# Kernel tuning notes

Hardware: AMD Instinct MI355X
Metric: run time of the kernel (lower is better)

Reference implementation:

```python
import jax, jax.numpy as jnp
import numpy as np

ALPHA = 0.5      # APPNP teleport prob (AG_EAGCN alpha=0.5)
DEPTH = 3        # APPNP depth
PROP_NUMS = 3    # EAGCN propagation steps


def _adj_process(adj, eps):
    # adj[adj<eps]=0 ; symmetrize ; add I ; D^-1/2 A D^-1/2 (inf->0)
    N = adj.shape[1]
    adj = jnp.where(adj < eps, 0.0, adj)
    adj = 0.5 * (adj + jnp.swapaxes(adj, 1, 2))
    adj = adj + jnp.eye(N, dtype=adj.dtype)
    d = jnp.sum(adj, axis=2)                                   # [n, N]
    dinv = jnp.where(d > 0, 1.0 / jnp.sqrt(jnp.where(d > 0, d, 1.0)), 0.0)
    return adj * dinv[:, :, None] * dinv[:, None, :]


def _eagcn(seg, edge, ws1, bs1, ws11, bs11, ws2, bs2, ws3, bs3, wmlp, bmlp, wgcn, bgcn):
    n, c, h, w = seg.shape
    hw = h * w
    num_s = ws1.shape[0]
    # conv_s1 (1x1)
    seg_s = jnp.einsum('nchw,sc->nshw', seg, ws1) + bs1[None, :, None, None]
    theta_T = seg_s.reshape(n, num_s, hw)       # raw view, as in torch
    theta = seg_s.reshape(n, hw, num_s)         # raw view (NOT transpose)
    # channel attention: diag_channel_att = ca ca^T is rank-1 ->
    # theta @ (ca ca^T) @ theta_T = (theta@ca) outer (ca@theta_T)
    pooled = seg.mean(axis=(2, 3))                              # [n, c]
    ca = jax.nn.relu(pooled @ wmlp.T + bmlp)                    # [n, num_s]
    u = jnp.einsum('nps,ns->np', theta, ca)                     # [n, hw]
    v = jnp.einsum('ns,nsq->nq', ca, theta_T)                   # [n, hw]
    sim_c = _adj_process(u[:, :, None] * v[:, None, :], 0.15)
    # spatial branch
    seg_c = jnp.einsum('nchw,sc->nshw', seg, ws11) + bs11[None, :, None, None]
    sigma = seg_c.reshape(n, num_s, hw)
    sigma_T = seg_c.reshape(n, hw, num_s)
    sigma_out = jnp.einsum('nps,nsq->npq', sigma_T, sigma)      # [n, hw, hw]
    edge_m = seg * edge
    seg_ss = (ws2 * seg.max(axis=1) + bs2).reshape(n, 1, hw)    # 1x1 conv on 1 chan
    edge_mm = (ws3 * edge_m.max(axis=1) + bs3).reshape(n, hw, 1)
    sim_s = _adj_process(sigma_out * (edge_mm * seg_ss), 0.15)
    sim = _adj_process(sim_c + sim_s, 0.0)
    # GCN_layer: relu(conv1d(seg @ sim)) + seg, residual
    seg2 = seg.reshape(n, c, hw)
    seg_sim = jnp.einsum('nck,nkq->ncq', seg2, sim)
    out = jax.nn.relu(jnp.einsum('oc,ncq->noq', wgcn, seg_sim) + bgcn[None, :, None]) + seg2
    return out.reshape(n, c, h, w), sim


def _appnp(seg, adj, wa1, ba1, wa2, ba2):
    n, c, h, w = seg.shape
    x = seg.reshape(n, h * w, c)                                # raw view
    t = jax.nn.relu(jax.nn.relu(x @ wa1.T + ba1) @ wa2.T + ba2)
    out = t
    for _ in range(DEPTH):
        out = (1.0 - ALPHA) * jnp.einsum('npq,nqc->npc', adj, out) + ALPHA * t
    return out


def _forward(seg, edge, ws1, bs1, ws11, bs11, ws2, bs2, ws3, bs3,
             wmlp, bmlp, wgcn, bgcn, wa1, ba1, wa2, ba2):
    ori = seg
    n, c, h, w = seg.shape
    adjs = []
    for _ in range(PROP_NUMS):
        seg, adj = _eagcn(seg, edge, ws1, bs1, ws11, bs11, ws2, bs2, ws3, bs3,
                          wmlp, bmlp, wgcn, bgcn)
        adjs.append(adj)
    adj = (adjs[0] + adjs[1] + adjs[2]) / float(PROP_NUMS)      # mean aggregation
    adj = _adj_process(adj, 0.0)
    # graph regularizer
    dirichlet = jnp.einsum('nii->', adj)                        # sum of traces
    N = adj.shape[1]
    gamma = 0.1; beta = 0.1; alpha_r = 0.1
    rowsum = jnp.sum(adj, axis=2)                               # adj @ ones
    f_A = (-beta * jnp.sum(jnp.log(rowsum), axis=1)[:, None, None] / N
           + gamma * jnp.sqrt(jnp.sum(adj * adj)) / (N ** 2))
    reg = alpha_r * dirichlet + f_A                             # [n,1,1]
    out = _appnp(ori, adj, wa1, ba1, wa2, ba2).reshape(n, c, h, w)
    return out, reg


def setup_inputs() -> dict:
    key = jax.random.key(0)
    ks = jax.random.split(key, 10)
    n, c, h, w = 8, 256, 32, 32
    num_s, hid = 64, 3

    def lin(k, out_f, in_f):
        lim = 1.0 / np.sqrt(in_f)
        return jax.random.uniform(k, (out_f, in_f), jnp.float32, -lim, lim)

    return dict(
        seg=jax.random.normal(ks[0], (n, c, h, w), jnp.float32),
        edge=jax.random.uniform(ks[1], (n, c, h, w), jnp.float32),
        ws1=lin(ks[2], num_s, c), bs1=jnp.zeros((num_s,), jnp.float32),
        ws11=lin(ks[3], num_s, c), bs11=jnp.zeros((num_s,), jnp.float32),
        ws2=jnp.asarray(0.7, jnp.float32), bs2=jnp.asarray(0.1, jnp.float32),
        ws3=jnp.asarray(0.6, jnp.float32), bs3=jnp.asarray(0.1, jnp.float32),
        wmlp=lin(ks[4], num_s, c), bmlp=jnp.zeros((num_s,), jnp.float32),
        wgcn=lin(ks[5], c, c), bgcn=jnp.zeros((c,), jnp.float32),
        wa1=lin(ks[6], hid, c), ba1=jnp.zeros((hid,), jnp.float32),
        wa2=lin(ks[7], c, hid), ba2=jnp.zeros((c,), jnp.float32),
    )


def reference(seg, edge, ws1, bs1, ws11, bs11, ws2, bs2, ws3, bs3,
              wmlp, bmlp, wgcn, bgcn, wa1, ba1, wa2, ba2):
    return _forward(seg, edge, ws1, bs1, ws11, bs11, ws2, bs2, ws3, bs3,
                    wmlp, bmlp, wgcn, bgcn, wa1, ba1, wa2, ba2)
```

## Files before the change

kernel.cpp:

```cpp
#include <hip/hip_runtime.h>
#include <math.h>

#define NB 8
#define C 256
#define HW 1024
#define NS 64

typedef unsigned short u16;
typedef __attribute__((ext_vector_type(8))) short bf16x8;
typedef __attribute__((ext_vector_type(4))) float f32x4;

__device__ __forceinline__ u16 f2bf(float x) {
    union { float f; unsigned u; } v; v.f = x;
    unsigned r = v.u + 0x7fffu + ((v.u >> 16) & 1u);
    return (u16)(r >> 16);
}
__device__ __forceinline__ float bf2f(u16 h) {
    union { unsigned u; float f; } v; v.u = ((unsigned)h) << 16; return v.f;
}
__device__ __forceinline__ void splitbf(float x, u16& h, u16& l) {
    h = f2bf(x);
    l = f2bf(x - bf2f(h));
}

__device__ __forceinline__ float blockReduceSum(float v, float* s4) {
    #pragma unroll
    for (int o = 32; o; o >>= 1) v += __shfl_down(v, o);
    __syncthreads();
    if ((threadIdx.x & 63) == 0) s4[threadIdx.x >> 6] = v;
    __syncthreads();
    return s4[0] + s4[1] + s4[2] + s4[3];
}

__global__ void k_presplit(const float* __restrict__ in, u16* __restrict__ oh,
                           u16* __restrict__ ol, int nElem) {
    for (int i = blockIdx.x * 256 + threadIdx.x; i < nElem; i += gridDim.x * 256) {
        u16 h, l; splitbf(in[i], h, l);
        oh[i] = h; ol[i] = l;
    }
}

__global__ void k_prepw(const float* __restrict__ ws1, const float* __restrict__ bs1,
                        const float* __restrict__ ws11, const float* __restrict__ bs11,
                        u16* __restrict__ WCH, u16* __restrict__ WCL, float* __restrict__ BCAT) {
    int tid = blockIdx.x * 256 + threadIdx.x;
    if (tid < 64 * C) {
        u16 h, l;
        splitbf(ws1[tid], h, l);  WCH[tid] = h;          WCL[tid] = l;
        splitbf(ws11[tid], h, l); WCH[64 * C + tid] = h; WCL[64 * C + tid] = l;
    }
    if (tid < 64) { BCAT[tid] = bs1[tid]; BCAT[64 + tid] = bs11[tid]; }
}

template<int R, int CIN, bool WF32>
__global__ void k_transp_split(const float* __restrict__ in, long long sIn,
                               u16* __restrict__ oh, u16* __restrict__ ol,
                               float* __restrict__ of, long long sOut) {
    int ti = blockIdx.x, tj = blockIdx.y, n = blockIdx.z, tid = threadIdx.x;
    int i0 = ti * 64, j0 = tj * 64;
    const float* ib = in + (size_t)n * sIn;
    __shared__ float L[64][65];
    for (int idx = tid; idx < 4096; idx += 256) {
        int r = idx >> 6, c = idx & 63;
        L[r][c] = ib[(size_t)(i0 + r) * CIN + (j0 + c)];
    }
    __syncthreads();
    for (int idx = tid; idx < 4096; idx += 256) {
        int r = idx >> 6, c = idx & 63;
        size_t o = (size_t)n * sOut + (size_t)(j0 + r) * R + (i0 + c);
        float val = L[c][r];
        u16 h, l; splitbf(val, h, l);
        oh[o] = h; ol[o] = l;
        if (WF32) of[o] = val;
    }
}

__global__ void k_pooled(const float* __restrict__ seg, float* __restrict__ pooled) {
    int c = blockIdx.x, n = blockIdx.y, tid = threadIdx.x;
    const float* row = seg + ((size_t)n * C + c) * HW;
    float acc = row[tid] + row[tid + 256] + row[tid + 512] + row[tid + 768];
    __shared__ float s4[4];
    float r = blockReduceSum(acc, s4);
    if (tid == 0) pooled[n * C + c] = r * (1.0f / HW);
}

__global__ void k_ca(const float* __restrict__ pooled, const float* __restrict__ wmlp,
                     const float* __restrict__ bmlp, float* __restrict__ ca) {
    int n = blockIdx.x, s = threadIdx.x;
    __shared__ float pl[C];
    for (int i = s; i < C; i += 64) pl[i] = pooled[n * C + i];
    __syncthreads();
    float acc = 0.f;
    for (int c = 0; c < C; ++c) acc += pl[c] * wmlp[s * C + c];
    float r = acc + bmlp[s];
    ca[n * NS + s] = r > 0.f ? r : 0.f;
}

__global__ void k_maxes(const float* __restrict__ seg, const float* __restrict__ edge,
                        float* __restrict__ smax, float* __restrict__ emax) {
    int pos = blockIdx.x * 256 + threadIdx.x;
    int n = blockIdx.y, ch = blockIdx.z;
    const float* sb = seg + (size_t)n * C * HW + (size_t)(ch * 32) * HW + pos;
    const float* eb = edge + (size_t)n * C * HW + (size_t)(ch * 32) * HW + pos;
    float ms = -3.402823466e38f, me = -3.402823466e38f;
    #pragma unroll 8
    for (int c = 0; c < 32; ++c) {
        float s = sb[(size_t)c * HW];
        ms = fmaxf(ms, s);
        me = fmaxf(me, s * eb[(size_t)c * HW]);
    }
    smax[((size_t)ch * NB + n) * HW + pos] = ms;
    emax[((size_t)ch * NB + n) * HW + pos] = me;
}

__global__ void k_maxfin(const float* __restrict__ smax, const float* __restrict__ emax,
                         const float* __restrict__ ws2, const float* __restrict__ bs2,
                         const float* __restrict__ ws3, const float* __restrict__ bs3,
                         float* __restrict__ segss, float* __restrict__ edgemm) {
    int pos = blockIdx.x * 256 + threadIdx.x;
    int n = blockIdx.y;
    float ms = -3.402823466e38f, me = -3.402823466e38f;
    #pragma unroll
    for (int ch = 0; ch < 8; ++ch) {
        ms = fmaxf(ms, smax[((size_t)ch * NB + n) * HW + pos]);
        me = fmaxf(me, emax[((size_t)ch * NB + n) * HW + pos]);
    }
    segss[n * HW + pos] = ws2[0] * ms + bs2[0];
    edgemm[n * HW + pos] = ws3[0] * me + bs3[0];
}

__global__ void k_uv(const float* __restrict__ segsc, const float* __restrict__ ca,
                     float* __restrict__ u, float* __restrict__ vv) {
    int pos = blockIdx.x * 256 + threadIdx.x;
    int n = blockIdx.y, role = blockIdx.z;
    const float* flat = segsc + (size_t)n * 128 * HW;
    __shared__ float cs[NS];
    if (threadIdx.x < NS) cs[threadIdx.x] = ca[n * NS + threadIdx.x];
    __syncthreads();
    if (role == 0) {
        const float* base = flat + (size_t)pos * NS;
        float acc = 0.f;
        #pragma unroll
        for (int s = 0; s < NS; ++s) acc += base[s] * cs[s];
        u[n * HW + pos] = acc;
    } else {
        float acc = 0.f;
        #pragma unroll
        for (int s = 0; s < NS; ++s) acc += cs[s] * flat[(size_t)s * HW + pos];
        vv[n * HW + pos] = acc;
    }
}

__global__ __launch_bounds__(256) void k_bbuild(
    const u16* __restrict__ AH, const u16* __restrict__ AL, long long sA,
    const u16* __restrict__ CTH, const u16* __restrict__ CTL, long long sCT,
    const float* __restrict__ em, const float* __restrict__ ss,
    float* __restrict__ B, float* __restrict__ dsum) {
    constexpr int LDK = 72;
    constexpr int TSZ = 64 * LDK;
    __shared__ __align__(16) u16 sm[4 * 2 * TSZ];
    int pi = blockIdx.x, n = blockIdx.y, tid = threadIdx.x;
    int i = 0, base = 0;
    while (pi >= base + (16 - i)) { base += 16 - i; ++i; }
    int j = i + (pi - base);
    int i0 = i * 64, j0 = j * 64;
    bool diag = (i == j);
    const u16* AnH = AH + (size_t)n * sA;
    const u16* AnL = AL + (size_t)n * sA;
    const u16* CnH = CTH + (size_t)n * sCT;
    const u16* CnL = CTL + (size_t)n * sCT;
    const float* emn = em + n * HW;
    const float* ssn = ss + n * HW;
    float* Bn = B + (size_t)n * HW * HW;

    auto stage = [&](int t, const u16* srcH, const u16* srcL, int r0) {
        u16* hi = sm + t * 2 * TSZ;
        u16* lo = hi + TSZ;
        #pragma unroll
        for (int p = 0; p < 2; ++p) {
            int e = (p * 256 + tid) * 8;
            int r = e >> 6, k0 = e & 63;
            size_t off = (size_t)(r0 + r) * 64 + k0;
            int b = r * LDK + k0;
            *(bf16x8*)(hi + b) = *(const bf16x8*)(srcH + off);
            *(bf16x8*)(lo + b) = *(const bf16x8*)(srcL + off);
        }
    };
    stage(0, AnH, AnL, i0);
    stage(2, CnH, CnL, i0);
    if (!diag) { stage(1, AnH, AnL, j0); stage(3, CnH, CnL, j0); }
    __syncthreads();

    int lane = tid & 63, wv = tid >> 6;
    int g = lane >> 4;
    f32x4 acc1[4], acc2[4];
    #pragma unroll
    for (int ni = 0; ni < 4; ++ni) {
        acc1[ni] = (f32x4){0.f, 0.f, 0.f, 0.f};
        acc2[ni] = (f32x4){0.f, 0.f, 0.f, 0.f};
    }

    const u16* AiH = sm + 0 * 2 * TSZ; const u16* AiL = AiH + TSZ;
    const u16* AjH = sm + 1 * 2 * TSZ; const u16* AjL = AjH + TSZ;
    const u16* BiH = sm + 2 * 2 * TSZ; const u16* BiL = BiH + TSZ;
    const u16* BjH = sm + 3 * 2 * TSZ; const u16* BjL = BjH + TSZ;

    #pragma unroll
    for (int kk = 0; kk < 2; ++kk) {
        int kl = kk * 32 + g * 8;
        int arow = wv * 16 + (lane & 15);
        bf16x8 a1h = *(const bf16x8*)(AiH + arow * LDK + kl);
        bf16x8 a1l = *(const bf16x8*)(AiL + arow * LDK + kl);
        bf16x8 a2h, a2l;
        if (!diag) {
            a2h = *(const bf16x8*)(AjH + arow * LDK + kl);
            a2l = *(const bf16x8*)(AjL + arow * LDK + kl);
        }
        #pragma unroll
        for (int ni = 0; ni < 4; ++ni) {
            int brow = ni * 16 + (lane & 15);
            if (diag) {
                bf16x8 bh = *(const bf16x8*)(BiH + brow * LDK + kl);
                bf16x8 bl = *(const bf16x8*)(BiL + brow * LDK + kl);
                acc1[ni] = __builtin_amdgcn_mfma_f32_16x16x32_bf16(a1h, bh, acc1[ni], 0, 0, 0);
                acc1[ni] = __builtin_amdgcn_mfma_f32_16x16x32_bf16(a1h, bl, acc1[ni], 0, 0, 0);
                acc1[ni] = __builtin_amdgcn_mfma_f32_16x16x32_bf16(a1l, bh, acc1[ni], 0, 0, 0);
            } else {
                bf16x8 b1h = *(const bf16x8*)(BjH + brow * LDK + kl);
                bf16x8 b1l = *(const bf16x8*)(BjL + brow * LDK + kl);
                acc1[ni] = __builtin_amdgcn_mfma_f32_16x16x32_bf16(a1h, b1h, acc1[ni], 0, 0, 0);
                acc1[ni] = __builtin_amdgcn_mfma_f32_16x16x32_bf16(a1h, b1l, acc1[ni], 0, 0, 0);
                acc1[ni] = __builtin_amdgcn_mfma_f32_16x16x32_bf16(a1l, b1h, acc1[ni], 0, 0, 0);
                bf16x8 b2h = *(const bf16x8*)(BiH + brow * LDK + kl);
                bf16x8 b2l = *(const bf16x8*)(BiL + brow * LDK + kl);
                acc2[ni] = __builtin_amdgcn_mfma_f32_16x16x32_bf16(a2h, b2h, acc2[ni], 0, 0, 0);
                acc2[ni] = __builtin_amdgcn_mfma_f32_16x16x32_bf16(a2h, b2l, acc2[ni], 0, 0, 0);
                acc2[ni] = __builtin_amdgcn_mfma_f32_16x16x32_bf16(a2l, b2h, acc2[ni], 0, 0, 0);
            }
        }
    }
    __syncthreads();

    float* t1 = (float*)sm;
    float* t2 = t1 + 64 * 65;
    float x[4][4], y[4][4];
    #pragma unroll
    for (int ni = 0; ni < 4; ++ni) {
        int col = ni * 16 + (lane & 15);
        #pragma unroll
        for (int r = 0; r < 4; ++r) {
            int row = wv * 16 + g * 4 + r;
            float v1 = acc1[ni][r] * emn[i0 + row] * ssn[j0 + col];
            v1 = v1 < 0.15f ? 0.f : v1;
            x[ni][r] = v1;
            t1[row * 65 + col] = v1;
            if (!diag) {
                float v2 = acc2[ni][r] * emn[j0 + row] * ssn[i0 + col];
                v2 = v2 < 0.15f ? 0.f : v2;
                y[ni][r] = v2;
                t2[row * 65 + col] = v2;
            }
        }
    }
    __syncthreads();

    float rs1[4] = {0.f, 0.f, 0.f, 0.f}, rs2[4] = {0.f, 0.f, 0.f, 0.f};
    #pragma unroll
    for (int ni = 0; ni < 4; ++ni) {
        int col = ni * 16 + (lane & 15);
        #pragma unroll
        for (int r = 0; r < 4; ++r) {
            int row = wv * 16 + g * 4 + r;
            float s1 = 0.5f * (x[ni][r] + (diag ? t1[col * 65 + row] : t2[col * 65 + row]));
            Bn[(size_t)(i0 + row) * HW + j0 + col] = s1;
            rs1[r] += s1;
            if (!diag) {
                float s2 = 0.5f * (y[ni][r] + t1[col * 65 + row]);
                Bn[(size_t)(j0 + row) * HW + i0 + col] = s2;
                rs2[r] += s2;
            }
        }
    }
    #pragma unroll
    for (int r = 0; r < 4; ++r) {
        #pragma unroll
        for (int m = 1; m < 16; m <<= 1) {
            rs1[r] += __shfl_xor(rs1[r], m);
            rs2[r] += __shfl_xor(rs2[r], m);
        }
    }
    if ((lane & 15) == 0) {
        #pragma unroll
        for (int r = 0; r < 4; ++r) {
            int row = wv * 16 + g * 4 + r;
            atomicAdd(&dsum[n * HW + i0 + row], rs1[r]);
            if (!diag) atomicAdd(&dsum[n * HW + j0 + row], rs2[r]);
        }
    }
}

template<int BM, int BN, int MODE>
__global__ __launch_bounds__(256) void k_mfma3(
    const u16* __restrict__ AH, const u16* __restrict__ AL, long long sA, int lda,
    const u16* __restrict__ BH, const u16* __restrict__ BL, long long sB, int ldb,
    int K,
    float* __restrict__ Cf, u16* __restrict__ CH, u16* __restrict__ CL,
    long long sC, int ldc,
    const float* __restrict__ e1,
    const float* __restrict__ e2, long long se2) {
    constexpr int WM = BM / 32;
    constexpr int WN = BN / 32;
    constexpr int LDK = 72;
    __shared__ __align__(16) u16 sAH[BM * LDK], sAL[BM * LDK];
    __shared__ __align__(16) u16 sBH[BN * LDK], sBL[BN * LDK];
    int n = blockIdx.z;
    int q0 = blockIdx.x * BN, m0 = blockIdx.y * BM;
    int tid = threadIdx.x, lane = tid & 63, wv = tid >> 6;
    int wm = wv >> 1, wn = wv & 1;

    f32x4 acc[WM][WN];
    #pragma unroll
    for (int mi = 0; mi < WM; ++mi)
        #pragma unroll
        for (int ni = 0; ni < WN; ++ni)
            acc[mi][ni] = (f32x4){0.f, 0.f, 0.f, 0.f};

    for (int kt = 0; kt < K; kt += 64) {
        #pragma unroll
        for (int p = 0; p < BM / 32; ++p) {
            int e = (p * 256 + tid) * 8;
            int r = e >> 6, k0 = e & 63;
            size_t off = (size_t)n * sA + (size_t)(m0 + r) * lda + kt + k0;
            int b = r * LDK + k0;
            *(bf16x8*)(sAH + b) = *(const bf16x8*)(AH + off);
            *(bf16x8*)(sAL + b) = *(const bf16x8*)(AL + off);
        }
        #pragma unroll
        for (int p = 0; p < BN / 32; ++p) {
            int e = (p * 256 + tid) * 8;
            int c = e >> 6, k0 = e & 63;
            size_t off = (size_t)n * sB + (size_t)(q0 + c) * ldb + kt + k0;
            int b = c * LDK + k0;
            *(bf16x8*)(sBH + b) = *(const bf16x8*)(BH + off);
            *(bf16x8*)(sBL + b) = *(const bf16x8*)(BL + off);
        }
        __syncthreads();
        #pragma unroll
        for (int kk = 0; kk < 2; ++kk) {
            int klocal = kk * 32 + (lane >> 4) * 8;
            bf16x8 aH[WM], aL[WM], bH[WN], bL[WN];
            #pragma unroll
            for (int mi = 0; mi < WM; ++mi) {
                int row = (wm * WM + mi) * 16 + (lane & 15);
                aH[mi] = *(const bf16x8*)(sAH + row * LDK + klocal);
                aL[mi] = *(const bf16x8*)(sAL + row * LDK + klocal);
            }
            #pragma unroll
            for (int ni = 0; ni < WN; ++ni) {
                int col = (wn * WN + ni) * 16 + (lane & 15);
                bH[ni] = *(const bf16x8*)(sBH + col * LDK + klocal);
                bL[ni] = *(const bf16x8*)(sBL + col * LDK + klocal);
            }
            #pragma unroll
            for (int mi = 0; mi < WM; ++mi)
                #pragma unroll
                for (int ni = 0; ni < WN; ++ni) {
                    acc[mi][ni] = __builtin_amdgcn_mfma_f32_16x16x32_bf16(aH[mi], bH[ni], acc[mi][ni], 0, 0, 0);
                    acc[mi][ni] = __builtin_amdgcn_mfma_f32_16x16x32_bf16(aH[mi], bL[ni], acc[mi][ni], 0, 0, 0);
                    acc[mi][ni] = __builtin_amdgcn_mfma_f32_16x16x32_bf16(aL[mi], bH[ni], acc[mi][ni], 0, 0, 0);
                }
        }
        __syncthreads();
    }

    #pragma unroll
    for (int mi = 0; mi < WM; ++mi) {
        #pragma unroll
        for (int ni = 0; ni < WN; ++ni) {
            int col = q0 + (wn * WN + ni) * 16 + (lane & 15);
            int rowb = m0 + (wm * WM + mi) * 16 + (lane >> 4) * 4;
            #pragma unroll
            for (int r = 0; r < 4; ++r) {
                int row = rowb + r;
                float val = acc[mi][ni][r];
                if (MODE == 0) {
                    u16 h, l; splitbf(val, h, l);
                    size_t o = (size_t)n * sC + (size_t)col * ldc + row;
                    CH[o] = h; CL[o] = l;
                } else if (MODE == 2) {
                    val = fmaxf(val + e1[row], 0.f) + e2[(size_t)n * se2 + (size_t)row * ldc + col];
                    size_t o = (size_t)n * sC + (size_t)row * ldc + col;
                    Cf[o] = val;
                    u16 h, l; splitbf(val, h, l);
                    CH[o] = h; CL[o] = l;
                } else if (MODE == 3) {
                    val = 0.5f * val + 0.5f * e2[(size_t)n * se2 + (size_t)row * ldc + col];
                    size_t o = (size_t)n * sC + (size_t)row * ldc + col;
                    u16 h, l; splitbf(val, h, l);
                    CH[o] = h; CL[o] = l;
                } else if (MODE == 4) {
                    val = 0.5f * val + 0.5f * e2[(size_t)n * se2 + (size_t)row * HW + col];
                    Cf[(size_t)n * sC + (size_t)col * ldc + row] = val;
                } else {
                    val = val + e1[row];
                    size_t o = (size_t)n * sC + (size_t)row * ldc + col;
                    Cf[o] = val;
                    u16 h, l; splitbf(val, h, l);
                    CH[o] = h; CL[o] = l;
                }
            }
        }
    }
}

__global__ void k_dinv(const float* __restrict__ u, const float* __restrict__ vv,
                       const float* __restrict__ dsum,
                       float* __restrict__ dcinv, float* __restrict__ dsinv) {
    int p = blockIdx.x, n = blockIdx.y, tid = threadIdx.x;
    const float* un = u + n * HW;
    const float* vn = vv + n * HW;
    float up = un[p], vp = vn[p];
    float acc_c = 0.f;
    for (int q = tid; q < HW; q += 256) {
        float x = up * vn[q]; x = x < 0.15f ? 0.f : x;
        float y = un[q] * vp; y = y < 0.15f ? 0.f : y;
        acc_c += 0.5f * (x + y);
    }
    __shared__ float s4[4];
    acc_c = blockReduceSum(acc_c, s4);
    if (tid == 0) {
        dcinv[n * HW + p] = 1.0f / sqrtf(acc_c + 1.0f);
        dsinv[n * HW + p] = 1.0f / sqrtf(dsum[n * HW + p] + 1.0f);
    }
}

__global__ void k_simsum(const float* __restrict__ B, const float* __restrict__ u,
                         const float* __restrict__ vv, const float* __restrict__ dcinv,
                         const float* __restrict__ dsinv, float* __restrict__ dfinv) {
    int p = blockIdx.x, n = blockIdx.y, tid = threadIdx.x;
    const float* Bb = B + (size_t)n * HW * HW + (size_t)p * HW;
    const float* un = u + n * HW;
    const float* vn = vv + n * HW;
    const float* dci = dcinv + n * HW;
    const float* dsi = dsinv + n * HW;
    float up = un[p], vp = vn[p], dcp = dci[p], dsp = dsi[p];
    float acc = 0.f;
    for (int q = tid; q < HW; q += 256) {
        float x = up * vn[q]; x = x < 0.15f ? 0.f : x;
        float y = un[q] * vp; y = y < 0.15f ? 0.f : y;
        float delta = (q == p) ? 1.0f : 0.0f;
        float val = (0.5f * (x + y) + delta) * dcp * dci[q] + (Bb[q] + delta) * dsp * dsi[q];
        acc += val;
    }
    __shared__ float s4[4];
    acc = blockReduceSum(acc, s4);
    if (tid == 0) dfinv[n * HW + p] = 1.0f / sqrtf(acc + 1.0f);
}

__global__ void k_norm_accum(const float* __restrict__ B, const float* __restrict__ u,
                             const float* __restrict__ vv, const float* __restrict__ dcinv,
                             const float* __restrict__ dsinv, const float* __restrict__ dfinv,
                             u16* __restrict__ SMH, u16* __restrict__ SML,
                             float* __restrict__ ACC, int first) {
    int p = blockIdx.x, n = blockIdx.y, tid = threadIdx.x;
    const float* Bb = B + (size_t)n * HW * HW + (size_t)p * HW;
    u16* Sh = SMH + (size_t)n * HW * HW + (size_t)p * HW;
    u16* Sl = SML + (size_t)n * HW * HW + (size_t)p * HW;
    float* Ab = ACC + (size_t)n * HW * HW + (size_t)p * HW;
    const float* un = u + n * HW;
    const float* vn = vv + n * HW;
    const float* dci = dcinv + n * HW;
    const float* dsi = dsinv + n * HW;
    const float* df = dfinv + n * HW;
    float up = un[p], vp = vn[p], dcp = dci[p], dsp = dsi[p], dfp = df[p];
    for (int q = tid; q < HW; q += 256) {
        float x = up * vn[q]; x = x < 0.15f ? 0.f : x;
        float y = un[q] * vp; y = y < 0.15f ? 0.f : y;
        float delta = (q == p) ? 1.0f : 0.0f;
        float sim_pre = (0.5f * (x + y) + delta) * dcp * dci[q] + (Bb[q] + delta) * dsp * dsi[q];
        float val = (sim_pre + delta) * dfp * df[q];
        u16 h, l; splitbf(val, h, l);
        Sh[q] = h; Sl[q] = l;
        Ab[q] = first ? val : (Ab[q] + val);
    }
}

__global__ void k_final_rowsum(const float* __restrict__ ACC, float* __restrict__ dinv) {
    int p = blockIdx.x, n = blockIdx.y, tid = threadIdx.x;
    const float* Ab = ACC + (size_t)n * HW * HW + (size_t)p * HW;
    float acc = 0.f;
    for (int q = tid; q < HW; q += 256) acc += Ab[q];
    __shared__ float s4[4];
    acc = blockReduceSum(acc, s4);
    if (tid == 0) dinv[n * HW + p] = 1.0f / sqrtf(acc * (1.0f / 3.0f) + 1.0f);
}

__global__ void k_final_norm(const float* __restrict__ ACC, const float* __restrict__ dinv,
                             u16* __restrict__ ADJH, u16* __restrict__ ADJL,
                             float* __restrict__ rowsf, float* __restrict__ diagrow,
                             float* __restrict__ sqrow) {
    int p = blockIdx.x, n = blockIdx.y, tid = threadIdx.x;
    const float* Ab = ACC + (size_t)n * HW * HW + (size_t)p * HW;
    u16* Oh = ADJH + (size_t)n * HW * HW + (size_t)p * HW;
    u16* Ol = ADJL + (size_t)n * HW * HW + (size_t)p * HW;
    const float* di = dinv + n * HW;
    float dp = di[p];
    float accr = 0.f, accsq = 0.f, accd = 0.f;
    for (int q = tid; q < HW; q += 256) {
        float val = (Ab[q] * (1.0f / 3.0f) + ((q == p) ? 1.f : 0.f)) * dp * di[q];
        u16 h, l; splitbf(val, h, l);
        Oh[q] = h; Ol[q] = l;
        accr += val;
        accsq += val * val;
        if (q == p) accd = val;
    }
    __shared__ float s4[4];
    accr = blockReduceSum(accr, s4);
    accsq = blockReduceSum(accsq, s4);
    accd = blockReduceSum(accd, s4);
    if (tid == 0) {
        rowsf[n * HW + p] = accr;
        sqrow[n * HW + p] = accsq;
        diagrow[n * HW + p] = accd;
    }
}

__global__ void k_scal(const float* __restrict__ diagrow, const float* __restrict__ sqrow,
                       float* __restrict__ scal) {
    int tid = threadIdx.x;
    float a = 0.f, b = 0.f;
    for (int i = tid; i < NB * HW; i += 256) { a += diagrow[i]; b += sqrow[i]; }
    __shared__ float s4[4];
    a = blockReduceSum(a, s4);
    b = blockReduceSum(b, s4);
    if (tid == 0) { scal[0] = a; scal[1] = b; }
}

__global__ void k_reg(const float* __restrict__ rowsf, const float* __restrict__ scal,
                      float* __restrict__ outreg) {
    int n = blockIdx.x, tid = threadIdx.x;
    float acc = 0.f;
    for (int p = tid; p < HW; p += 256) acc += logf(rowsf[n * HW + p]);
    __shared__ float s4[4];
    acc = blockReduceSum(acc, s4);
    if (tid == 0) {
        float f = -0.1f * acc / 1024.0f + 0.1f * sqrtf(scal[1]) / 1048576.0f;
        outreg[n] = 0.1f * scal[0] + f;
    }
}

__global__ void k_appnp_t(const float* __restrict__ ori, const float* __restrict__ wa1,
                          const float* __restrict__ ba1, const float* __restrict__ wa2,
                          const float* __restrict__ ba2, float* __restrict__ T) {
    int p = blockIdx.x, n = blockIdx.y, tid = threadIdx.x;
    const float* x = ori + (size_t)n * C * HW + (size_t)p * C;
    float xv = x[tid];
    __shared__ float s4[4];
    __shared__ float h[3];
    float d0 = blockReduceSum(xv * wa1[0 * C + tid], s4);
    float d1 = blockReduceSum(xv * wa1[1 * C + tid], s4);
    float d2 = blockReduceSum(xv * wa1[2 * C + tid], s4);
    if (tid == 0) {
        h[0] = fmaxf(d0 + ba1[0], 0.f);
        h[1] = fmaxf(d1 + ba1[1], 0.f);
        h[2] = fmaxf(d2 + ba1[2], 0.f);
    }
    __syncthreads();
    float t = h[0] * wa2[tid * 3 + 0] + h[1] * wa2[tid * 3 + 1] + h[2] * wa2[tid * 3 + 2] + ba2[tid];
    T[(size_t)n * HW * C + (size_t)p * C + tid] = fmaxf(t, 0.f);
}

extern "C" void kernel_launch(void* const* d_in, const int* in_sizes, int n_in,
                              void* d_out, int out_size, void* d_ws, size_t ws_size,
                              hipStream_t stream) {
    const float* seg_in = (const float*)d_in[0];
    const float* edge   = (const float*)d_in[1];
    const float* ws1    = (const float*)d_in[2];
    const float* bs1    = (const float*)d_in[3];
    const float* ws11   = (const float*)d_in[4];
    const float* bs11   = (const float*)d_in[5];
    const float* ws2    = (const float*)d_in[6];
    const float* bs2    = (const float*)d_in[7];
    const float* ws3    = (const float*)d_in[8];
    const float* bs3    = (const float*)d_in[9];
    const float* wmlp   = (const float*)d_in[10];
    const float* bmlp   = (const float*)d_in[11];
    const float* wgcn   = (const float*)d_in[12];
    const float* bgcn   = (const float*)d_in[13];
    const float* wa1    = (const float*)d_in[14];
    const float* ba1    = (const float*)d_in[15];
    const float* wa2    = (const float*)d_in[16];
    const float* ba2    = (const float*)d_in[17];

    float* out = (float*)d_out;
    char* wb = (char*)d_ws;
    size_t off = 0;
    auto nf = [&](size_t elems) -> float* {
        float* p = (float*)(wb + off); off += ((elems * 4 + 255) & ~(size_t)255); return p; };
    auto nu = [&](size_t elems) -> u16* {
        u16* p = (u16*)(wb + off); off += ((elems * 2 + 255) & ~(size_t)255); return p; };

    float* SEG_A   = nf((size_t)NB * C * HW);
    float* SEGSC   = nf((size_t)NB * 128 * HW);
    float* TT      = nf((size_t)NB * C * HW);
    float* TBUF    = nf((size_t)NB * HW * C);
    float* BBUF    = nf((size_t)NB * HW * HW);
    float* ACCUM   = nf((size_t)NB * HW * HW);
    float* MAXS    = nf((size_t)8 * NB * HW);
    float* MAXE    = nf((size_t)8 * NB * HW);
    float* BCAT    = nf(128);
    float* ubuf    = nf(NB * HW);
    float* vbuf    = nf(NB * HW);
    float* ssbuf   = nf(NB * HW);
    float* embuf   = nf(NB * HW);
    float* dsum    = nf(NB * HW);
    float* dcinv   = nf(NB * HW);
    float* dsinv   = nf(NB * HW);
    float* dfinv   = nf(NB * HW);
    float* rowsf   = nf(NB * HW);
    float* diagrow = nf(NB * HW);
    float* sqrow   = nf(NB * HW);
    float* pooled  = nf(NB * C);
    float* cabuf   = nf(NB * NS);
    float* scal    = nf(16);
    u16* SAH  = nu((size_t)NB * C * HW);   u16* SAL  = nu((size_t)NB * C * HW);
    u16* TGH  = nu((size_t)NB * HW * C);   u16* TGL  = nu((size_t)NB * HW * C);
    u16* WCH  = nu((size_t)128 * C);       u16* WCL  = nu((size_t)128 * C);
    u16* WGH  = nu((size_t)C * C);         u16* WGL  = nu((size_t)C * C);
    u16* SCH  = nu((size_t)NB * 128 * HW); u16* SCL  = nu((size_t)NB * 128 * HW);
    u16* CTH  = nu((size_t)NB * HW * NS);  u16* CTL  = nu((size_t)NB * HW * NS);
    u16* SMH  = nu((size_t)NB * HW * HW);  u16* SML  = nu((size_t)NB * HW * HW);
    u16* SIMTH= nu((size_t)NB * HW * C);   u16* SIMTL= nu((size_t)NB * HW * C);
    u16* TTH  = nu((size_t)NB * C * HW);   u16* TTL  = nu((size_t)NB * C * HW);
    u16* X1H  = nu((size_t)NB * C * HW);   u16* X1L  = nu((size_t)NB * C * HW);
    u16* X2H  = nu((size_t)NB * C * HW);   u16* X2L  = nu((size_t)NB * C * HW);
    u16* ADJH = SMH;
    u16* ADJL = SML;

    const long long sAdj = (long long)HW * HW;
    const long long sSeg = (long long)C * HW;
    const long long sSC  = (long long)128 * HW;
    const long long sCT  = (long long)HW * NS;

    k_prepw<<<dim3(64), 256, 0, stream>>>(ws1, bs1, ws11, bs11, WCH, WCL, BCAT);
    k_presplit<<<dim3(64), 256, 0, stream>>>(wgcn, WGH, WGL, C * C);
    k_presplit<<<dim3(2048), 256, 0, stream>>>(seg_in, SAH, SAL, NB * C * HW);

    for (int it = 0; it < 3; ++it) {
        const float* seg_src = (it == 0) ? seg_in : SEG_A;
        k_transp_split<C, HW, false><<<dim3(4, 16, NB), 256, 0, stream>>>(
            seg_src, sSeg, TGH, TGL, nullptr, sSeg);
        k_mfma3<64, 64, 5><<<dim3(16, 2, NB), 256, 0, stream>>>(
            WCH, WCL, 0, C, TGH, TGL, sSeg, C, C,
            SEGSC, SCH, SCL, sSC, HW, BCAT, nullptr, 0);
        k_transp_split<NS, HW, false><<<dim3(1, 16, NB), 256, 0, stream>>>(
            SEGSC + (size_t)64 * HW, sSC, CTH, CTL, nullptr, sCT);
        k_pooled<<<dim3(C, NB), 256, 0, stream>>>(seg_src, pooled);
        k_ca<<<dim3(NB), 64, 0, stream>>>(pooled, wmlp, bmlp, cabuf);
        k_maxes<<<dim3(4, NB, 8), 256, 0, stream>>>(seg_src, edge, MAXS, MAXE);
        k_maxfin<<<dim3(4, NB), 256, 0, stream>>>(MAXS, MAXE, ws2, bs2, ws3, bs3, ssbuf, embuf);
        k_uv<<<dim3(4, NB, 2), 256, 0, stream>>>(SEGSC, cabuf, ubuf, vbuf);
        hipMemsetAsync(dsum, 0, (size_t)NB * HW * sizeof(float), stream);
        k_bbuild<<<dim3(136, NB), 256, 0, stream>>>(
            SCH + (size_t)64 * HW, SCL + (size_t)64 * HW, sSC,
            CTH, CTL, sCT, embuf, ssbuf, BBUF, dsum);
        k_dinv<<<dim3(HW, NB), 256, 0, stream>>>(ubuf, vbuf, dsum, dcinv, dsinv);
        k_simsum<<<dim3(HW, NB), 256, 0, stream>>>(BBUF, ubuf, vbuf, dcinv, dsinv, dfinv);
        k_norm_accum<<<dim3(HW, NB), 256, 0, stream>>>(BBUF, ubuf, vbuf, dcinv, dsinv, dfinv,
                                                       SMH, SML, ACCUM, it == 0 ? 1 : 0);
        k_mfma3<64, 64, 0><<<dim3(16, 4, NB), 256, 0, stream>>>(
            SAH, SAL, sSeg, HW, SMH, SML, sAdj, HW, HW,
            nullptr, SIMTH, SIMTL, sSeg, C, nullptr, nullptr, 0);
        k_mfma3<64, 64, 2><<<dim3(16, 4, NB), 256, 0, stream>>>(
            WGH, WGL, 0, C, SIMTH, SIMTL, sSeg, C, C,
            SEG_A, SAH, SAL, sSeg, HW, bgcn, seg_src, sSeg);
    }

    k_final_rowsum<<<dim3(HW, NB), 256, 0, stream>>>(ACCUM, dcinv);
    k_final_norm<<<dim3(HW, NB), 256, 0, stream>>>(ACCUM, dcinv, ADJH, ADJL, rowsf, diagrow, sqrow);
    k_scal<<<dim3(1), 256, 0, stream>>>(diagrow, sqrow, scal);
    k_reg<<<dim3(NB), 256, 0, stream>>>(rowsf, scal, out + (size_t)NB * C * HW);

    k_appnp_t<<<dim3(HW, NB), 256, 0, stream>>>(seg_in, wa1, ba1, wa2, ba2, TBUF);
    k_transp_split<HW, C, true><<<dim3(16, 4, NB), 256, 0, stream>>>(
        TBUF, sSeg, TTH, TTL, TT, sSeg);
    k_mfma3<64, 64, 3><<<dim3(16, 4, NB), 256, 0, stream>>>(
        TTH, TTL, sSeg, HW, ADJH, ADJL, sAdj, HW, HW,
        nullptr, X1H, X1L, sSeg, HW, nullptr, TT, sSeg);
    k_mfma3<64, 64, 3><<<dim3(16, 4, NB), 256, 0, stream>>>(
        X1H, X1L, sSeg, HW, ADJH, ADJL, sAdj, HW, HW,
        nullptr, X2H, X2L, sSeg, HW, nullptr, TT, sSeg);
    k_mfma3<64, 64, 4><<<dim3(16, 4, NB), 256, 0, stream>>>(
        X2H, X2L, sSeg, HW, ADJH, ADJL, sAdj, HW, HW,
        out, nullptr, nullptr, sSeg, C, nullptr, TT, sSeg);
}
```

Baseline: 583.9 us.

## Stage transposed GEMM epilogues through LDS, shrink tiles, fold memset and scal kernel

Transposed-store epilogues (MODE 0 and 4) now write the tile into shared memory first, then store it to global memory in column-contiguous order. This replaces the strided scattered 2-byte and 4-byte writes. GEMM tiles shrink from 64x64 to 32x64, doubling the block count for better occupancy on the small grids. The dsum memset is folded into k_maxfin and k_scal is merged into k_reg to remove launches, at the cost of extra LDS traffic and a sync in the epilogue.

```diff
diff --git a/kernel.cpp b/kernel.cpp
--- a/kernel.cpp
+++ b/kernel.cpp
@@ -116,7 +116,8 @@
 __global__ void k_maxfin(const float* __restrict__ smax, const float* __restrict__ emax,
                          const float* __restrict__ ws2, const float* __restrict__ bs2,
                          const float* __restrict__ ws3, const float* __restrict__ bs3,
-                         float* __restrict__ segss, float* __restrict__ edgemm) {
+                         float* __restrict__ segss, float* __restrict__ edgemm,
+                         float* __restrict__ dsum) {
     int pos = blockIdx.x * 256 + threadIdx.x;
     int n = blockIdx.y;
     float ms = -3.402823466e38f, me = -3.402823466e38f;
@@ -127,6 +128,7 @@
     }
     segss[n * HW + pos] = ws2[0] * ms + bs2[0];
     edgemm[n * HW + pos] = ws3[0] * me + bs3[0];
+    dsum[n * HW + pos] = 0.f;
 }
 
 __global__ void k_uv(const float* __restrict__ segsc, const float* __restrict__ ca,
@@ -311,8 +313,11 @@
     constexpr int WM = BM / 32;
     constexpr int WN = BN / 32;
     constexpr int LDK = 72;
-    __shared__ __align__(16) u16 sAH[BM * LDK], sAL[BM * LDK];
-    __shared__ __align__(16) u16 sBH[BN * LDK], sBL[BN * LDK];
+    __shared__ __align__(16) u16 smem[(BM + BN) * LDK * 2];
+    u16* sAH = smem;
+    u16* sAL = smem + BM * LDK;
+    u16* sBH = smem + 2 * BM * LDK;
+    u16* sBL = smem + 2 * BM * LDK + BN * LDK;
     int n = blockIdx.z;
     int q0 = blockIdx.x * BN, m0 = blockIdx.y * BM;
     int tid = threadIdx.x, lane = tid & 63, wv = tid >> 6;
@@ -373,40 +378,81 @@
         __syncthreads();
     }
 
-    #pragma unroll
-    for (int mi = 0; mi < WM; ++mi) {
-        #pragma unroll
-        for (int ni = 0; ni < WN; ++ni) {
-            int col = q0 + (wn * WN + ni) * 16 + (lane & 15);
-            int rowb = m0 + (wm * WM + mi) * 16 + (lane >> 4) * 4;
+    if (MODE == 0) {
+        u16* Th = smem;
+        u16* Tl = smem + BN * (BM + 1);
+        #pragma unroll
+        for (int mi = 0; mi < WM; ++mi) {
             #pragma unroll
-            for (int r = 0; r < 4; ++r) {
-                int row = rowb + r;
-                float val = acc[mi][ni][r];
-                if (MODE == 0) {
-                    u16 h, l; splitbf(val, h, l);
-                    size_t o = (size_t)n * sC + (size_t)col * ldc + row;
-                    CH[o] = h; CL[o] = l;
-                } else if (MODE == 2) {
-                    val = fmaxf(val + e1[row], 0.f) + e2[(size_t)n * se2 + (size_t)row * ldc + col];
-                    size_t o = (size_t)n * sC + (size_t)row * ldc + col;
-                    Cf[o] = val;
-                    u16 h, l; splitbf(val, h, l);
-                    CH[o] = h; CL[o] = l;
-                } else if (MODE == 3) {
-                    val = 0.5f * val + 0.5f * e2[(size_t)n * se2 + (size_t)row * ldc + col];
-                    size_t o = (size_t)n * sC + (size_t)row * ldc + col;
-                    u16 h, l; splitbf(val, h, l);
-                    CH[o] = h; CL[o] = l;
-                } else if (MODE == 4) {
-                    val = 0.5f * val + 0.5f * e2[(size_t)n * se2 + (size_t)row * HW + col];
-                    Cf[(size_t)n * sC + (size_t)col * ldc + row] = val;
-                } else {
-                    val = val + e1[row];
-                    size_t o = (size_t)n * sC + (size_t)row * ldc + col;
-                    Cf[o] = val;
-                    u16 h, l; splitbf(val, h, l);
-                    CH[o] = h; CL[o] = l;
+            for (int ni = 0; ni < WN; ++ni) {
+                int cl = (wn * WN + ni) * 16 + (lane & 15);
+                int rb = (wm * WM + mi) * 16 + (lane >> 4) * 4;
+                #pragma unroll
+                for (int r = 0; r < 4; ++r) {
+                    u16 h, l; splitbf(acc[mi][ni][r], h, l);
+                    Th[cl * (BM + 1) + rb + r] = h;
+                    Tl[cl * (BM + 1) + rb + r] = l;
+                }
+            }
+        }
+        __syncthreads();
+        for (int idx = tid; idx < BM * BN; idx += 256) {
+            int q = idx / BM, m = idx % BM;
+            size_t o = (size_t)n * sC + (size_t)(q0 + q) * ldc + (m0 + m);
+            CH[o] = Th[q * (BM + 1) + m];
+            CL[o] = Tl[q * (BM + 1) + m];
+        }
+    } else if (MODE == 4) {
+        float* Tf = (float*)smem;
+        #pragma unroll
+        for (int mi = 0; mi < WM; ++mi) {
+            #pragma unroll
+            for (int ni = 0; ni < WN; ++ni) {
+                int cl = (wn * WN + ni) * 16 + (lane & 15);
+                int rb = (wm * WM + mi) * 16 + (lane >> 4) * 4;
+                #pragma unroll
+                for (int r = 0; r < 4; ++r) {
+                    int row = m0 + rb + r, col = q0 + cl;
+                    float val = 0.5f * acc[mi][ni][r]
+                              + 0.5f * e2[(size_t)n * se2 + (size_t)row * HW + col];
+                    Tf[cl * (BM + 1) + rb + r] = val;
+                }
+            }
+        }
+        __syncthreads();
+        for (int idx = tid; idx < BM * BN; idx += 256) {
+            int q = idx / BM, m = idx % BM;
+            Cf[(size_t)n * sC + (size_t)(q0 + q) * ldc + (m0 + m)] = Tf[q * (BM + 1) + m];
+        }
+    } else {
+        #pragma unroll
+        for (int mi = 0; mi < WM; ++mi) {
+            #pragma unroll
+            for (int ni = 0; ni < WN; ++ni) {
+                int col = q0 + (wn * WN + ni) * 16 + (lane & 15);
+                int rowb = m0 + (wm * WM + mi) * 16 + (lane >> 4) * 4;
+                #pragma unroll
+                for (int r = 0; r < 4; ++r) {
+                    int row = rowb + r;
+                    float val = acc[mi][ni][r];
+                    if (MODE == 2) {
+                        val = fmaxf(val + e1[row], 0.f) + e2[(size_t)n * se2 + (size_t)row * ldc + col];
+                        size_t o = (size_t)n * sC + (size_t)row * ldc + col;
+                        Cf[o] = val;
+                        u16 h, l; splitbf(val, h, l);
+                        CH[o] = h; CL[o] = l;
+                    } else if (MODE == 3) {
+                        val = 0.5f * val + 0.5f * e2[(size_t)n * se2 + (size_t)row * ldc + col];
+                        size_t o = (size_t)n * sC + (size_t)row * ldc + col;
+                        u16 h, l; splitbf(val, h, l);
+                        CH[o] = h; CL[o] = l;
+                    } else {
+                        val = val + e1[row];
+                        size_t o = (size_t)n * sC + (size_t)row * ldc + col;
+                        Cf[o] = val;
+                        u16 h, l; splitbf(val, h, l);
+                        CH[o] = h; CL[o] = l;
+                    }
                 }
             }
         }
@@ -525,27 +571,19 @@
     }
 }
 
-__global__ void k_scal(const float* __restrict__ diagrow, const float* __restrict__ sqrow,
-                       float* __restrict__ scal) {
-    int tid = threadIdx.x;
-    float a = 0.f, b = 0.f;
+__global__ void k_reg(const float* __restrict__ rowsf, const float* __restrict__ diagrow,
+                      const float* __restrict__ sqrow, float* __restrict__ outreg) {
+    int n = blockIdx.x, tid = threadIdx.x;
+    float acc = 0.f, a = 0.f, b = 0.f;
+    for (int p = tid; p < HW; p += 256) acc += logf(rowsf[n * HW + p]);
     for (int i = tid; i < NB * HW; i += 256) { a += diagrow[i]; b += sqrow[i]; }
     __shared__ float s4[4];
+    acc = blockReduceSum(acc, s4);
     a = blockReduceSum(a, s4);
     b = blockReduceSum(b, s4);
-    if (tid == 0) { scal[0] = a; scal[1] = b; }
-}
-
-__global__ void k_reg(const float* __restrict__ rowsf, const float* __restrict__ scal,
-                      float* __restrict__ outreg) {
-    int n = blockIdx.x, tid = threadIdx.x;
-    float acc = 0.f;
-    for (int p = tid; p < HW; p += 256) acc += logf(rowsf[n * HW + p]);
-    __shared__ float s4[4];
-    acc = blockReduceSum(acc, s4);
     if (tid == 0) {
-        float f = -0.1f * acc / 1024.0f + 0.1f * sqrtf(scal[1]) / 1048576.0f;
-        outreg[n] = 0.1f * scal[0] + f;
+        float f = -0.1f * acc / 1024.0f + 0.1f * sqrtf(b) / 1048576.0f;
+        outreg[n] = 0.1f * a + f;
     }
 }
 
@@ -636,6 +674,7 @@
     u16* X2H  = nu((size_t)NB * C * HW);   u16* X2L  = nu((size_t)NB * C * HW);
     u16* ADJH = SMH;
     u16* ADJL = SML;
+    (void)scal;
 
     const long long sAdj = (long long)HW * HW;
     const long long sSeg = (long long)C * HW;
@@ -650,7 +689,7 @@
         const float* seg_src = (it == 0) ? seg_in : SEG_A;
         k_transp_split<C, HW, false><<<dim3(4, 16, NB), 256, 0, stream>>>(
             seg_src, sSeg, TGH, TGL, nullptr, sSeg);
-        k_mfma3<64, 64, 5><<<dim3(16, 2, NB), 256, 0, stream>>>(
+        k_mfma3<32, 64, 5><<<dim3(16, 4, NB), 256, 0, stream>>>(
             WCH, WCL, 0, C, TGH, TGL, sSeg, C, C,
             SEGSC, SCH, SCL, sSC, HW, BCAT, nullptr, 0);
         k_transp_split<NS, HW, false><<<dim3(1, 16, NB), 256, 0, stream>>>(
@@ -658,9 +697,9 @@
         k_pooled<<<dim3(C, NB), 256, 0, stream>>>(seg_src, pooled);
         k_ca<<<dim3(NB), 64, 0, stream>>>(pooled, wmlp, bmlp, cabuf);
         k_maxes<<<dim3(4, NB, 8), 256, 0, stream>>>(seg_src, edge, MAXS, MAXE);
-        k_maxfin<<<dim3(4, NB), 256, 0, stream>>>(MAXS, MAXE, ws2, bs2, ws3, bs3, ssbuf, embuf);
+        k_maxfin<<<dim3(4, NB), 256, 0, stream>>>(MAXS, MAXE, ws2, bs2, ws3, bs3,
+                                                  ssbuf, embuf, dsum);
         k_uv<<<dim3(4, NB, 2), 256, 0, stream>>>(SEGSC, cabuf, ubuf, vbuf);
-        hipMemsetAsync(dsum, 0, (size_t)NB * HW * sizeof(float), stream);
         k_bbuild<<<dim3(136, NB), 256, 0, stream>>>(
             SCH + (size_t)64 * HW, SCL + (size_t)64 * HW, sSC,
             CTH, CTL, sCT, embuf, ssbuf, BBUF, dsum);
@@ -668,29 +707,28 @@
         k_simsum<<<dim3(HW, NB), 256, 0, stream>>>(BBUF, ubuf, vbuf, dcinv, dsinv, dfinv);
         k_norm_accum<<<dim3(HW, NB), 256, 0, stream>>>(BBUF, ubuf, vbuf, dcinv, dsinv, dfinv,
                                                        SMH, SML, ACCUM, it == 0 ? 1 : 0);
-        k_mfma3<64, 64, 0><<<dim3(16, 4, NB), 256, 0, stream>>>(
+        k_mfma3<32, 64, 0><<<dim3(16, 8, NB), 256, 0, stream>>>(
             SAH, SAL, sSeg, HW, SMH, SML, sAdj, HW, HW,
             nullptr, SIMTH, SIMTL, sSeg, C, nullptr, nullptr, 0);
-        k_mfma3<64, 64, 2><<<dim3(16, 4, NB), 256, 0, stream>>>(
+        k_mfma3<32, 64, 2><<<dim3(16, 8, NB), 256, 0, stream>>>(
             WGH, WGL, 0, C, SIMTH, SIMTL, sSeg, C, C,
             SEG_A, SAH, SAL, sSeg, HW, bgcn, seg_src, sSeg);
     }
 
     k_final_rowsum<<<dim3(HW, NB), 256, 0, stream>>>(ACCUM, dcinv);
     k_final_norm<<<dim3(HW, NB), 256, 0, stream>>>(ACCUM, dcinv, ADJH, ADJL, rowsf, diagrow, sqrow);
-    k_scal<<<dim3(1), 256, 0, stream>>>(diagrow, sqrow, scal);
-    k_reg<<<dim3(NB), 256, 0, stream>>>(rowsf, scal, out + (size_t)NB * C * HW);
+    k_reg<<<dim3(NB), 256, 0, stream>>>(rowsf, diagrow, sqrow, out + (size_t)NB * C * HW);
 
     k_appnp_t<<<dim3(HW, NB), 256, 0, stream>>>(seg_in, wa1, ba1, wa2, ba2, TBUF);
     k_transp_split<HW, C, true><<<dim3(16, 4, NB), 256, 0, stream>>>(
         TBUF, sSeg, TTH, TTL, TT, sSeg);
-    k_mfma3<64, 64, 3><<<dim3(16, 4, NB), 256, 0, stream>>>(
+    k_mfma3<32, 64, 3><<<dim3(16, 8, NB), 256, 0, stream>>>(
         TTH, TTL, sSeg, HW, ADJH, ADJL, sAdj, HW, HW,
         nullptr, X1H, X1L, sSeg, HW, nullptr, TT, sSeg);
-    k_mfma3<64, 64, 3><<<dim3(16, 4, NB), 256, 0, stream>>>(
+    k_mfma3<32, 64, 3><<<dim3(16, 8, NB), 256, 0, stream>>>(
         X1H, X1L, sSeg, HW, ADJH, ADJL, sAdj, HW, HW,
         nullptr, X2H, X2L, sSeg, HW, nullptr, TT, sSeg);
-    k_mfma3<64, 64, 4><<<dim3(16, 4, NB), 256, 0, stream>>>(
+    k_mfma3<32, 64, 4><<<dim3(16, 8, NB), 256, 0, stream>>>(
         X2H, X2L, sSeg, HW, ADJH, ADJL, sAdj, HW, HW,
         out, nullptr, nullptr, sSeg, C, nullptr, TT, sSeg);
 }
```

Result: slower. 606.1 us (+3.8%).
